# Kernel tuning notes

Measured on AMD Instinct MI355X. Metric: run time of the kernel, lower is better.

The kernel has to match this reference:

```python
import jax, jax.numpy as jnp
import numpy as np

B, Z, L = 256, 256, 8
C0, H0, W0 = 128, 8, 8
O = C0 * H0 * W0  # 8192


def _conv_transpose(x, w, b):
    """Torch ConvTranspose2d(k=4, s=2, p=1) equivalent.
    w: torch layout (in_ch, out_ch, kH, kW).
    Implemented as lhs-dilated conv with flipped, transposed kernel; pad = k-1-p = 2.
    """
    wt = jnp.flip(w, (2, 3)).transpose(1, 0, 2, 3)  # (out, in, kh, kw)
    y = jax.lax.conv_general_dilated(
        x, wt, window_strides=(1, 1), padding=[(2, 2), (2, 2)],
        lhs_dilation=(2, 2), dimension_numbers=('NCHW', 'OIHW', 'NCHW'))
    return y + b[None, :, None, None]


def setup_inputs() -> dict:
    key = jax.random.key(0)
    ks = jax.random.split(key, 6)
    return {
        'x': jax.random.normal(ks[0], (B, Z), jnp.float32),
        'gw': jax.random.normal(ks[1], (Z, L), jnp.float32) * (2.0 / (Z + L)) ** 0.5,  # xavier_normal
        'gb': jnp.zeros((L,), jnp.float32),
        'pw': jax.random.normal(ks[2], (O, Z, L), jnp.float32) * (1.0 / Z) ** 0.5,  # kaiming linear
        'pb': jnp.zeros((O, L), jnp.float32),
        'w1': jax.random.normal(ks[3], (C0, 64, 4, 4), jnp.float32) * 0.02,
        'b1': jnp.zeros((64,), jnp.float32),
        'w2': jax.random.normal(ks[4], (64, 32, 4, 4), jnp.float32) * 0.02,
        'b2': jnp.zeros((32,), jnp.float32),
        'w3': jax.random.normal(ks[5], (32, 3, 4, 4), jnp.float32) * 0.02,
        'b3': jnp.zeros((3,), jnp.float32),
    }


def reference(x, gw, gb, pw, pb, w1, b1, w2, b2, w3, b3):
    # --- ME mixture of linear experts (linear projection) ---
    g = jax.nn.softmax(x @ gw + gb, axis=1)               # (B, L)
    # Per-expert linear outputs, then gate-weighted sum. Mathematically equal to
    # torch's (pw @ gatings) per-sample weight followed by bmm with x, but avoids
    # the (B, O, Z) intermediate.
    expert_out = jnp.einsum('bi,oil->bol', x, pw)          # (B, O, L)
    out = jnp.einsum('bol,bl->bo', expert_out, g) + g @ pb.T  # (B, O)
    # --- conv-transpose decoder stack ---
    h = out.reshape(B, C0, H0, W0)
    h = jax.nn.relu(_conv_transpose(h, w1, b1))            # (B, 64, 16, 16)
    h = jax.nn.relu(_conv_transpose(h, w2, b2))            # (B, 32, 32, 32)
    h = _conv_transpose(h, w3, b3)                         # (B, 3, 64, 64)
    return h
```

## Files before the change

kernel.cpp:

```cpp
#include <hip/hip_runtime.h>

typedef __bf16 bf16;
typedef __bf16 bf16x8 __attribute__((ext_vector_type(8)));
typedef float f32x4 __attribute__((ext_vector_type(4)));

__device__ __forceinline__ f32x4 mfma16(bf16x8 a, bf16x8 b, f32x4 c) {
  return __builtin_amdgcn_mfma_f32_16x16x32_bf16(a, b, c, 0, 0, 0);
}

__device__ __forceinline__ void gload16(const void* g, void* l) {
  __builtin_amdgcn_global_load_lds(
      (const __attribute__((address_space(1))) void*)g,
      (__attribute__((address_space(3))) void*)(uint32_t)(size_t)l, 16, 0, 0);
}

__device__ __forceinline__ bf16x8 cvt8(float4 a, float4 b) {
  bf16x8 r;
  r[0] = (bf16)a.x; r[1] = (bf16)a.y; r[2] = (bf16)a.z; r[3] = (bf16)a.w;
  r[4] = (bf16)b.x; r[5] = (bf16)b.y; r[6] = (bf16)b.z; r[7] = (bf16)b.w;
  return r;
}

template <int CIN, int COUT, int COUTP>
__device__ __forceinline__ void cw_one(const float* __restrict__ w,
                                       bf16* __restrict__ wp, int idx) {
  constexpr int K = 4 * CIN;
  int ic = idx & (CIN - 1);
  int t = (idx / CIN) & 3;
  int oc = (idx / K) % COUTP;
  int p = idx / (K * COUTP);
  bf16 v = (bf16)0.f;
  if (oc < COUT) {
    int py = p >> 1, px = p & 1, tyi = t >> 1, txi = t & 1;
    int ky = py == 0 ? (tyi ? 3 : 1) : (tyi ? 2 : 0);
    int kx = px == 0 ? (txi ? 3 : 1) : (txi ? 2 : 0);
    v = (bf16)w[((ic * COUT + oc) * 4 + ky) * 4 + kx];
  }
  wp[idx] = v;
}

template <int HP, int WP, int C>
__device__ __forceinline__ void bz_one(bf16* __restrict__ buf, int idx) {
  constexpr int NCELL = 2 * WP + 2 * (HP - 2);
  constexpr int C8 = C / 8;
  int c8 = idx % C8;
  int rem = idx / C8;
  int cell = rem % NCELL;
  int b = rem / NCELL;
  int y, x;
  if (cell < WP) { y = 0; x = cell; }
  else if (cell < 2 * WP) { y = HP - 1; x = cell - WP; }
  else { int r2 = cell - 2 * WP; y = 1 + (r2 >> 1); x = (r2 & 1) ? WP - 1 : 0; }
  bf16x8 z = {};
  *(bf16x8*)(buf + ((size_t)(b * HP + y) * WP + x) * C + c8 * 8) = z;
}

__global__ __launch_bounds__(256) void prep_kernel(
    const float* __restrict__ x, const float* __restrict__ gw,
    const float* __restrict__ gb, bf16* __restrict__ xgbP,
    float* __restrict__ gbuf,
    const float* __restrict__ w1, bf16* __restrict__ w1p,
    const float* __restrict__ w2, bf16* __restrict__ w2p,
    const float* __restrict__ w3, bf16* __restrict__ w3p,
    bf16* __restrict__ h0t, bf16* __restrict__ h1, bf16* __restrict__ h2) {
  __shared__ float xs[256];
  __shared__ float gs[8];
  const int bid = blockIdx.x, tid = threadIdx.x;
  if (bid < 256) {
    const int b = bid;
    xs[tid] = x[b * 256 + tid];
    __syncthreads();
    if (tid < 8) {
      float acc = gb[tid];
      for (int i = 0; i < 256; ++i) acc += xs[i] * gw[i * 8 + tid];
      gs[tid] = acc;
    }
    __syncthreads();
    if (tid == 0) {
      float m = gs[0];
      for (int l = 1; l < 8; ++l) m = fmaxf(m, gs[l]);
      float s = 0.f, e[8];
      for (int l = 0; l < 8; ++l) { e[l] = expf(gs[l] - m); s += e[l]; }
      float inv = 1.f / s;
      for (int l = 0; l < 8; ++l) gs[l] = e[l] * inv;
    }
    __syncthreads();
    if (tid < 8) gbuf[b * 8 + tid] = gs[tid];
    float xv = xs[tid];
    bf16x8 r;
#pragma unroll
    for (int j = 0; j < 8; ++j) r[j] = (bf16)(xv * gs[j]);
    size_t off = (size_t)(b >> 4) * 65536 + (size_t)(tid >> 2) * 1024 +
                 (size_t)(((tid & 3) * 16 + (b & 15)) * 16);
    *(bf16x8*)((char*)xgbP + off) = r;
  } else if (bid < 928) {
    int idx = (bid - 256) * 256 + tid;
    if (idx < 131072) cw_one<128, 64, 64>(w1, w1p, idx);
    else if (idx < 163840) cw_one<64, 32, 32>(w2, w2p, idx - 131072);
    else if (idx < 172032) cw_one<32, 3, 16>(w3, w3p, idx - 163840);
  } else {
    int idx = (bid - 928) * 256 + tid;
    if (idx < 147456) bz_one<10, 10, 128>(h0t, idx);
    else if (idx < 286720) bz_one<18, 18, 64>(h1, idx - 147456);
    else if (idx < 421888) bz_one<34, 34, 32>(h2, idx - 286720);
  }
}

__global__ __launch_bounds__(512) void me_gemm_kernel(
    const float* __restrict__ pw, const bf16* __restrict__ xgbP,
    const float* __restrict__ pb, const float* __restrict__ gbuf,
    bf16* __restrict__ h0t) {
  __shared__ char sA[32768];
  const int tid = threadIdx.x, wv = tid >> 6, l = tid & 63;
  const int lr = l & 15, lkg = l >> 4;
  const int M0 = blockIdx.x * 16;

  int aoff[2];
#pragma unroll
  for (int ks = 0; ks < 2; ++ks)
    aoff[ks] = lr * 128 + (((ks * 4 + lkg) * 16) ^ ((lr & 7) << 4));

  const char* pB0 = (const char*)xgbP + (size_t)(2 * wv) * 65536 + l * 16;
  const char* pB1 = (const char*)xgbP + (size_t)(2 * wv + 1) * 65536 + l * 16;

  f32x4 acc[2] = {};
#pragma unroll
  for (int ph = 0; ph < 2; ++ph) {
    if (ph) __syncthreads();
#pragma unroll
    for (int it = 0; it < 4; ++it) {
      int g = it * 512 + tid;
      int kt = g >> 7, rem = g & 127;
      int row = rem >> 3, ig = rem & 7;
      const float* src = pw + (size_t)(M0 + row) * 2048 + ph * 1024 + kt * 64 + ig * 8;
      float4 v0 = *(const float4*)src;
      float4 v1 = *(const float4*)(src + 4);
      int L = kt * 2048 + row * 128 + ((ig * 16) ^ ((row & 7) << 4));
      *(bf16x8*)(sA + L) = cvt8(v0, v1);
    }
    __syncthreads();
#pragma unroll 8
    for (int sl = 0; sl < 32; ++sl) {
      const int s = ph * 32 + sl;
      const char* base = sA + (sl >> 1) * 2048;
      bf16x8 a0 = *(const bf16x8*)(base + aoff[sl & 1]);
      bf16x8 b0 = *(const bf16x8*)(pB0 + s * 1024);
      bf16x8 b1 = *(const bf16x8*)(pB1 + s * 1024);
      acc[0] = mfma16(a0, b0, acc[0]);
      acc[1] = mfma16(a0, b1, acc[1]);
    }
  }

  float4 g0[2], g1[2];
#pragma unroll
  for (int n = 0; n < 2; ++n) {
    int b = wv * 32 + n * 16 + lr;
    g0[n] = *(const float4*)(gbuf + b * 8);
    g1[n] = *(const float4*)(gbuf + b * 8 + 4);
  }
#pragma unroll
  for (int r = 0; r < 4; ++r) {
    int o = M0 + lkg * 4 + r;
    float4 p0 = *(const float4*)(pb + o * 8);
    float4 p1 = *(const float4*)(pb + o * 8 + 4);
    int cch = o >> 6, y = (o >> 3) & 7, xx = o & 7;
#pragma unroll
    for (int n = 0; n < 2; ++n) {
      int b = wv * 32 + n * 16 + lr;
      float bias = g0[n].x * p0.x + g0[n].y * p0.y + g0[n].z * p0.z + g0[n].w * p0.w +
                   g1[n].x * p1.x + g1[n].y * p1.y + g1[n].z * p1.z + g1[n].w * p1.w;
      h0t[((size_t)(b * 10 + y + 1) * 10 + xx + 1) * 128 + cch] = (bf16)(acc[n][r] + bias);
    }
  }
}

template <int CIN, int H, int YB, int COUTP, int WM, int NF, int SWM,
          bool WLDS, int INIT, int WIT, bool RELU, bool F32OUT, int SIN_SZ, int SW_SZ>
__global__ __launch_bounds__(256) void convt_kernel(
    const bf16* __restrict__ in, const bf16* __restrict__ wp,
    const float* __restrict__ bias, bf16* __restrict__ out,
    float* __restrict__ fout) {
  constexpr int W = H, WROW = W + 2, ROWB = CIN * 2, GRS = ROWB / 16;
  constexpr int LGR = (GRS == 16) ? 4 : (GRS == 8) ? 3 : 2;
  constexpr int LW = (W == 8) ? 3 : (W == 16) ? 4 : 5;
  constexpr int K = 4 * CIN;
  constexpr int CHUNKS = (YB + 2) * WROW * GRS;
  constexpr int WGR = K / 8;
  __shared__ char sIn[SIN_SZ];
  __shared__ char sW[SW_SZ];

  const int tid = threadIdx.x, wv = tid >> 6, l = tid & 63;
  const int nyb = H / YB;
  const int img = blockIdx.x / nyb, y0 = (blockIdx.x % nyb) * YB;
  const int p = blockIdx.y, py = p >> 1, px = p & 1;

#pragma unroll
  for (int it = 0; it < INIT; ++it) {
    int t = it * 256 + tid;
    int tc = t < CHUNKS ? t : CHUNKS - 1;
    int pix = tc >> LGR, cc = tc & (GRS - 1);
    int ly = pix / WROW, lx = pix % WROW;
    int sb = (cc * 16) ^ ((pix & SWM) << 4);
    gload16(in + ((size_t)((img * (H + 2) + y0 + ly) * (W + 2) + lx)) * CIN + (sb >> 1),
            sIn + it * 4096 + wv * 1024);
  }
  if constexpr (WLDS) {
#pragma unroll
    for (int it = 0; it < WIT; ++it) {
      int t = it * 256 + tid;
      int oc = t / WGR, cc = t % WGR;
      int sb = (cc * 16) ^ ((oc & 7) << 4);
      gload16(wp + (size_t)(p * COUTP + oc) * K + (sb >> 1), sW + it * 4096 + wv * 1024);
    }
  }
  __syncthreads();

  const int lr = l & 15, lkg = l >> 4;
  const int wm = wv & (WM - 1), wn = wv / WM;
  int pcen[2];
#pragma unroll
  for (int m = 0; m < 2; ++m) {
    int r = wm * 32 + m * 16 + lr;
    pcen[m] = ((r >> LW) + 1) * WROW + (r & (W - 1)) + 1;
  }

  f32x4 acc[2][NF] = {};
#pragma unroll 4
  for (int kk = 0; kk < K; kk += 32) {
    const int t4 = kk / CIN;
    const int tyi = t4 >> 1, txi = t4 & 1;
    const int dy = (py == 0) ? (tyi ? -1 : 0) : (tyi ? 0 : 1);
    const int dx = (px == 0) ? (txi ? -1 : 0) : (txi ? 0 : 1);
    const int icb = (kk % CIN) * 2 + lkg * 16;
    bf16x8 av[2], bv[NF];
#pragma unroll
    for (int m = 0; m < 2; ++m) {
      int pixd = pcen[m] + dy * WROW + dx;
      av[m] = *(const bf16x8*)(sIn + pixd * ROWB + (icb ^ ((pixd & SWM) << 4)));
    }
#pragma unroll
    for (int n = 0; n < NF; ++n) {
      int oc = (wn * NF + n) * 16 + lr;
      if constexpr (WLDS) {
        int kb = kk * 2 + lkg * 16;
        bv[n] = *(const bf16x8*)(sW + oc * (K * 2) + (kb ^ ((oc & 7) << 4)));
      } else {
        bv[n] = *(const bf16x8*)(wp + (size_t)(p * COUTP + oc) * K + kk + lkg * 8);
      }
    }
#pragma unroll
    for (int m = 0; m < 2; ++m)
#pragma unroll
      for (int n = 0; n < NF; ++n) acc[m][n] = mfma16(av[m], bv[n], acc[m][n]);
  }

#pragma unroll
  for (int m = 0; m < 2; ++m)
#pragma unroll
    for (int r4 = 0; r4 < 4; ++r4) {
      int r = wm * 32 + m * 16 + lkg * 4 + r4;
      int yy = r >> LW, xx = r & (W - 1);
      int oy = 2 * (y0 + yy) + py, ox = 2 * xx + px;
#pragma unroll
      for (int n = 0; n < NF; ++n) {
        int oc = (wn * NF + n) * 16 + lr;
        float v = acc[m][n][r4];
        if constexpr (F32OUT) {
          if (oc < 3) fout[((size_t)(img * 3 + oc) * (2 * H) + oy) * (2 * H) + ox] = v + bias[oc];
        } else {
          v += bias[oc];
          if constexpr (RELU) v = fmaxf(v, 0.f);
          out[((size_t)(img * (2 * H + 2) + oy + 1) * (2 * H + 2) + ox + 1) * COUTP + oc] = (bf16)v;
        }
      }
    }
}

extern "C" void kernel_launch(void* const* d_in, const int* in_sizes, int n_in,
                              void* d_out, int out_size, void* d_ws, size_t ws_size,
                              hipStream_t stream) {
  const float* x  = (const float*)d_in[0];
  const float* gw = (const float*)d_in[1];
  const float* gb = (const float*)d_in[2];
  const float* pw = (const float*)d_in[3];
  const float* pb = (const float*)d_in[4];
  const float* w1 = (const float*)d_in[5];
  const float* b1 = (const float*)d_in[6];
  const float* w2 = (const float*)d_in[7];
  const float* b2 = (const float*)d_in[8];
  const float* w3 = (const float*)d_in[9];
  const float* b3 = (const float*)d_in[10];
  float* outp = (float*)d_out;

  char* ws = (char*)d_ws;
  bf16*  xgbP = (bf16*)(ws + 0);
  float* gbuf = (float*)(ws + 1048576);
  bf16*  h0t  = (bf16*)(ws + 1056768);
  bf16*  w1p  = (bf16*)(ws + 7610368);
  bf16*  h1   = (bf16*)(ws + 7872512);
  bf16*  w2p  = (bf16*)(ws + 18489344);
  bf16*  h2   = (bf16*)(ws + 18554880);
  bf16*  w3p  = (bf16*)(ws + 37494784);

  prep_kernel<<<2576, 256, 0, stream>>>(x, gw, gb, xgbP, gbuf,
                                        w1, w1p, w2, w2p, w3, w3p, h0t, h1, h2);

  me_gemm_kernel<<<512, 512, 0, stream>>>(pw, xgbP, pb, gbuf, h0t);

  convt_kernel<128, 8, 8, 64, 2, 2, 7, false, 7, 0, true, false, 28672, 16>
      <<<dim3(256, 4), 256, 0, stream>>>(h0t, w1p, b1, h1, nullptr);
  convt_kernel<64, 16, 8, 32, 4, 2, 7, true, 6, 4, true, false, 24576, 16384>
      <<<dim3(512, 4), 256, 0, stream>>>(h1, w2p, b2, h2, nullptr);
  convt_kernel<32, 32, 4, 16, 4, 1, 3, true, 4, 1, false, true, 16384, 4096>
      <<<dim3(2048, 4), 256, 0, stream>>>(h2, w3p, b3, nullptr, outp);
}
```

Before: 107.5 us.

## Stream B operand through per-wave LDS ring with async global-to-LDS prefetch

The ME GEMM kernel's B operand (xgbP) was read straight from global memory on each k-step. It is now staged through a 4-slot per-wave LDS ring using global_load_lds, prefetching three steps ahead and gated by explicit vmcnt waits. This aims to hide global load latency behind the MFMA work. In exchange LDS use grows from 32KB to 96KB per block, which may lower occupancy. The inline waitcnt sequencing is fragile because other vector-memory loads, such as the pw loads in phase 2, also count toward vmcnt.

```diff
diff --git a/kernel.cpp b/kernel.cpp
--- a/kernel.cpp
+++ b/kernel.cpp
@@ -12,6 +12,13 @@
   __builtin_amdgcn_global_load_lds(
       (const __attribute__((address_space(1))) void*)g,
       (__attribute__((address_space(3))) void*)(uint32_t)(size_t)l, 16, 0, 0);
+}
+
+template <int N> __device__ __forceinline__ void waitv() {
+  if constexpr (N == 4) asm volatile("s_waitcnt vmcnt(4)" ::: "memory");
+  else if constexpr (N == 2) asm volatile("s_waitcnt vmcnt(2)" ::: "memory");
+  else asm volatile("s_waitcnt vmcnt(0)" ::: "memory");
+  __builtin_amdgcn_sched_barrier(0);
 }
 
 __device__ __forceinline__ bf16x8 cvt8(float4 a, float4 b) {
@@ -110,7 +117,7 @@
     const float* __restrict__ pw, const bf16* __restrict__ xgbP,
     const float* __restrict__ pb, const float* __restrict__ gbuf,
     bf16* __restrict__ h0t) {
-  __shared__ char sA[32768];
+  __shared__ char sMem[98304];
   const int tid = threadIdx.x, wv = tid >> 6, l = tid & 63;
   const int lr = l & 15, lkg = l >> 4;
   const int M0 = blockIdx.x * 16;
@@ -122,30 +129,60 @@
 
   const char* pB0 = (const char*)xgbP + (size_t)(2 * wv) * 65536 + l * 16;
   const char* pB1 = (const char*)xgbP + (size_t)(2 * wv + 1) * 65536 + l * 16;
+  char* ring = sMem + 32768 + wv * 8192;
+
+#pragma unroll
+  for (int s0 = 0; s0 < 3; ++s0) {
+    gload16(pB0 + s0 * 1024, ring + s0 * 2048);
+    gload16(pB1 + s0 * 1024, ring + s0 * 2048 + 1024);
+  }
+#pragma unroll
+  for (int it = 0; it < 4; ++it) {
+    int g = it * 512 + tid;
+    int kt = g >> 7, rem = g & 127;
+    int row = rem >> 3, ig = rem & 7;
+    const float* src = pw + (size_t)(M0 + row) * 2048 + kt * 64 + ig * 8;
+    float4 v0 = *(const float4*)src;
+    float4 v1 = *(const float4*)(src + 4);
+    int L = kt * 2048 + row * 128 + ((ig * 16) ^ ((row & 7) << 4));
+    *(bf16x8*)(sMem + L) = cvt8(v0, v1);
+  }
+  __syncthreads();
 
   f32x4 acc[2] = {};
 #pragma unroll
   for (int ph = 0; ph < 2; ++ph) {
-    if (ph) __syncthreads();
-#pragma unroll
-    for (int it = 0; it < 4; ++it) {
-      int g = it * 512 + tid;
-      int kt = g >> 7, rem = g & 127;
-      int row = rem >> 3, ig = rem & 7;
-      const float* src = pw + (size_t)(M0 + row) * 2048 + ph * 1024 + kt * 64 + ig * 8;
-      float4 v0 = *(const float4*)src;
-      float4 v1 = *(const float4*)(src + 4);
-      int L = kt * 2048 + row * 128 + ((ig * 16) ^ ((row & 7) << 4));
-      *(bf16x8*)(sA + L) = cvt8(v0, v1);
-    }
-    __syncthreads();
-#pragma unroll 8
+    if (ph) {
+      __syncthreads();
+#pragma unroll
+      for (int it = 0; it < 4; ++it) {
+        int g = it * 512 + tid;
+        int kt = g >> 7, rem = g & 127;
+        int row = rem >> 3, ig = rem & 7;
+        const float* src = pw + (size_t)(M0 + row) * 2048 + 1024 + kt * 64 + ig * 8;
+        float4 v0 = *(const float4*)src;
+        float4 v1 = *(const float4*)(src + 4);
+        int L = kt * 2048 + row * 128 + ((ig * 16) ^ ((row & 7) << 4));
+        *(bf16x8*)(sMem + L) = cvt8(v0, v1);
+      }
+      __syncthreads();
+    }
+#pragma unroll
     for (int sl = 0; sl < 32; ++sl) {
       const int s = ph * 32 + sl;
-      const char* base = sA + (sl >> 1) * 2048;
-      bf16x8 a0 = *(const bf16x8*)(base + aoff[sl & 1]);
-      bf16x8 b0 = *(const bf16x8*)(pB0 + s * 1024);
-      bf16x8 b1 = *(const bf16x8*)(pB1 + s * 1024);
+      if (s <= 61) waitv<4>();
+      else if (s == 62) waitv<2>();
+      else waitv<0>();
+      const char* rb = ring + (s & 3) * 2048;
+      bf16x8 b0 = *(const bf16x8*)(rb + l * 16);
+      bf16x8 b1 = *(const bf16x8*)(rb + 1024 + l * 16);
+      const char* abase = sMem + (sl >> 1) * 2048;
+      bf16x8 a0 = *(const bf16x8*)(abase + aoff[sl & 1]);
+      if (s + 3 <= 63) {
+        char* wdst = ring + ((s + 3) & 3) * 2048;
+        gload16(pB0 + (s + 3) * 1024, wdst);
+        gload16(pB1 + (s + 3) * 1024, wdst + 1024);
+      }
       acc[0] = mfma16(a0, b0, acc[0]);
       acc[1] = mfma16(a0, b1, acc[1]);
     }
```

Result: faster. 104.2 us (-3.1%).
